# Kernel optimization log

Hardware: AMD Instinct MI355X
Metric: run time of the kernel (lower is better)

The kernel has to match this reference:

```python
import jax, jax.numpy as jnp
import numpy as np

LOCAL_RADIUS = 5


def setup_inputs() -> dict:
    key = jax.random.key(0)
    k1, k2, k3 = jax.random.split(key, 3)
    B, K, C, H = 4, 4096, 256, 128
    x = jax.random.normal(k1, (B, K, C), dtype=jnp.float32)
    W1 = jax.random.normal(k2, (C, H), dtype=jnp.float32) * (1.0 / np.sqrt(C))
    b1 = jnp.zeros((H,), dtype=jnp.float32)
    W2 = jax.random.normal(k3, (H, 1), dtype=jnp.float32) * (1.0 / np.sqrt(H))
    b2 = jnp.zeros((1,), dtype=jnp.float32)
    return {"x": x, "W1": W1, "b1": b1, "W2": W2, "b2": b2}


def reference(x, W1, b1, W2, b2):
    # x: [B, k, C]. The MLP score for column j is independent of the row i,
    # so compute it once per token instead of per (i, window) as in the torch loop.
    B, k, C = x.shape
    s = (jnp.tanh(x @ W1 + b1) @ W2 + b2)[..., 0]  # [B, k]
    idx = jnp.arange(k)
    band = (jnp.abs(idx[:, None] - idx[None, :]) <= LOCAL_RADIUS)  # [k, k]
    # Outside the band the original leaves scores at 0.0 (not -inf), so
    # out-of-window positions still contribute exp(0)=1 to the softmax.
    scores = jnp.where(band[None, :, :], s[:, None, :], jnp.float32(0.0))  # [B, k, k]
    weights = jax.nn.softmax(scores, axis=-1)  # [B, k, k]
    weighted = jnp.einsum('bij,bjc->bic', weights, x)  # [B, k, C]
    return weighted, weights
```

## Files before the change

kernel.cpp:

```cpp
#include <hip/hip_runtime.h>
#include <math.h>

#define B_ 4
#define K_ 4096
#define C_ 256
#define H_ 128
#define RAD 5
#define NB (2 * RAD + 1)
#define PSTRIDE 12

typedef float floatx4 __attribute__((ext_vector_type(4)));


__global__ __launch_bounds__(128) void score_kernel(
    const float* __restrict__ x, const float* __restrict__ W1,
    const float* __restrict__ b1, const float* __restrict__ W2,
    const float* __restrict__ b2, float* __restrict__ s_out)
{
    const int tid = threadIdx.x;
    const int t0 = blockIdx.x * 8;
    const float* xr[8];
    #pragma unroll
    for (int t = 0; t < 8; ++t) xr[t] = x + (size_t)(t0 + t) * C_;

    float acc[8];
    float binit = b1[tid];
    #pragma unroll
    for (int t = 0; t < 8; ++t) acc[t] = binit;

    for (int c = 0; c < C_; c += 4) {
        float w0 = W1[(c + 0) * H_ + tid];
        float w1 = W1[(c + 1) * H_ + tid];
        float w2 = W1[(c + 2) * H_ + tid];
        float w3 = W1[(c + 3) * H_ + tid];
        #pragma unroll
        for (int t = 0; t < 8; ++t) {
            floatx4 xv = *(const floatx4*)&xr[t][c];
            acc[t] = fmaf(xv.x, w0, acc[t]);
            acc[t] = fmaf(xv.y, w1, acc[t]);
            acc[t] = fmaf(xv.z, w2, acc[t]);
            acc[t] = fmaf(xv.w, w3, acc[t]);
        }
    }

    __shared__ float red[2][8];
    float w2v = W2[tid];
    #pragma unroll
    for (int t = 0; t < 8; ++t) {
        float p = tanhf(acc[t]) * w2v;
        #pragma unroll
        for (int off = 32; off > 0; off >>= 1) p += __shfl_down(p, off);
        if ((tid & 63) == 0) red[tid >> 6][t] = p;
    }
    __syncthreads();
    if (tid < 8) s_out[t0 + tid] = red[0][tid] + red[1][tid] + b2[0];
}

__global__ __launch_bounds__(256) void colsum_partial(
    const float* __restrict__ x, float* __restrict__ partial)
{
    const int tid = threadIdx.x;
    const int blk = blockIdx.x;
    const float* base = x + (size_t)blk * 32 * C_ + tid;
    float a0 = 0.f, a1 = 0.f, a2 = 0.f, a3 = 0.f;
    #pragma unroll
    for (int kk = 0; kk < 32; kk += 4) {
        a0 += base[(size_t)(kk + 0) * C_];
        a1 += base[(size_t)(kk + 1) * C_];
        a2 += base[(size_t)(kk + 2) * C_];
        a3 += base[(size_t)(kk + 3) * C_];
    }
    partial[(size_t)blk * C_ + tid] = (a0 + a1) + (a2 + a3);
}

__global__ __launch_bounds__(256) void colsum_final(
    const float* __restrict__ partial, float* __restrict__ Ssum)
{
    const int tid = threadIdx.x;
    const int b = blockIdx.x;
    float acc = 0.f;
    for (int chunk = 0; chunk < 128; ++chunk)
        acc += partial[(size_t)(b * 128 + chunk) * C_ + tid];
    Ssum[b * C_ + tid] = acc;
}

__global__ __launch_bounds__(256) void params_kernel(
    const float* __restrict__ s, float* __restrict__ params)
{
    const int row = blockIdx.x * 256 + threadIdx.x;
    const int b = row >> 12;
    const int i = row & (K_ - 1);
    const int j0 = max(0, i - RAD), j1 = min(K_ - 1, i + RAD);
    const int nb = j1 - j0 + 1;
    const float* srow = s + b * K_;

    float sv[NB];
    float m = 0.f;
    #pragma unroll
    for (int jj = 0; jj < NB; ++jj) {
        float v = (jj < nb) ? srow[j0 + jj] : 0.f;
        sv[jj] = v;
        if (jj < nb) m = fmaxf(m, v);
    }
    float e0 = expf(-m);
    float D = (float)(K_ - nb) * e0;
    float* pp = params + (size_t)row * PSTRIDE;
    #pragma unroll
    for (int jj = 0; jj < NB; ++jj) {
        float e = expf(sv[jj] - m);
        if (jj < nb) D += e;
        sv[jj] = e;
    }
    float inv = 1.0f / D;
    #pragma unroll
    for (int jj = 0; jj < NB; ++jj) pp[jj] = sv[jj] * inv;
    pp[11] = e0 * inv;
}

__global__ __launch_bounds__(256) void store_kernel(
    const float* __restrict__ x, const float* __restrict__ params,
    const float* __restrict__ Ssum, float* __restrict__ out)
{
    const int tid = threadIdx.x;
    const int row = blockIdx.x;
    const int b = row >> 12;
    const int i = row & (K_ - 1);
    const int j0 = max(0, i - RAD), j1 = min(K_ - 1, i + RAD);
    const int nb = j1 - j0 + 1;

    __shared__ float wbs[PSTRIDE];
    if (tid < PSTRIDE) wbs[tid] = params[(size_t)row * PSTRIDE + tid];
    __syncthreads();
    const float woff = wbs[11];

    {
        float acc = woff * Ssum[b * C_ + tid];
        const float* xb = x + ((size_t)b * K_ + j0) * C_ + tid;
        #pragma unroll
        for (int jj = 0; jj < NB; ++jj) {
            if (jj < nb)
                acc = fmaf(wbs[jj] - woff, xb[(size_t)jj * C_], acc);
        }
        out[(size_t)row * C_ + tid] = acc;
    }

    floatx4* wrow4 = (floatx4*)(out + (size_t)B_ * K_ * C_ + (size_t)row * K_);
    #pragma unroll
    for (int q = 0; q < 4; ++q) {
        const int f = tid + 256 * q;
        const int jb = f * 4;
        floatx4 v = { woff, woff, woff, woff };
        if (jb + 3 >= j0 && jb <= j1) {
            if (jb + 0 >= j0 && jb + 0 <= j1) v.x = wbs[jb + 0 - j0];
            if (jb + 1 >= j0 && jb + 1 <= j1) v.y = wbs[jb + 1 - j0];
            if (jb + 2 >= j0 && jb + 2 <= j1) v.z = wbs[jb + 2 - j0];
            if (jb + 3 >= j0 && jb + 3 <= j1) v.w = wbs[jb + 3 - j0];
        }
        __builtin_nontemporal_store(v, wrow4 + f);
    }
}

extern "C" void kernel_launch(void* const* d_in, const int* in_sizes, int n_in,
                              void* d_out, int out_size, void* d_ws, size_t ws_size,
                              hipStream_t stream) {
    const float* x  = (const float*)d_in[0];
    const float* W1 = (const float*)d_in[1];
    const float* b1 = (const float*)d_in[2];
    const float* W2 = (const float*)d_in[3];
    const float* b2 = (const float*)d_in[4];
    float* out = (float*)d_out;

    float* ws      = (float*)d_ws;
    float* s       = ws;
    float* Ssum    = ws + 16384;
    float* partial = ws + 17408;
    float* params  = ws + 148480;

    score_kernel  <<<B_ * K_ / 8,  128, 0, stream>>>(x, W1, b1, W2, b2, s);
    colsum_partial<<<B_ * 128,     256, 0, stream>>>(x, partial);
    colsum_final  <<<B_,           256, 0, stream>>>(partial, Ssum);
    params_kernel <<<B_ * K_ / 256,256, 0, stream>>>(s, params);
    store_kernel  <<<B_ * K_,      256, 0, stream>>>(x, params, Ssum, out);
}
```

Before: 380.3 us.

## Tile store kernel over 16 rows with shared x halo, parallelize colsum_final

The store kernel now handles 16 output rows per block. It stages the 26-token x window in shared memory once, so neighbouring rows reuse it instead of each re-reading 11 tokens from global memory. colsum_final goes from 256 to 1024 threads per block with a shared-memory reduction, shortening its serial loop. The weights matrix is now written with ordinary stores instead of nontemporal stores. That could change cache behaviour on the dominant 256 MB write stream and offset the savings.

Result: no change. 383.9 us (+0.9%).

```diff
diff --git a/kernel.cpp b/kernel.cpp
--- a/kernel.cpp
+++ b/kernel.cpp
@@ -8,6 +8,7 @@
 #define RAD 5
 #define NB (2 * RAD + 1)
 #define PSTRIDE 12
+#define TROWS 16
 
 typedef float floatx4 __attribute__((ext_vector_type(4)));
 
@@ -73,15 +74,20 @@
     partial[(size_t)blk * C_ + tid] = (a0 + a1) + (a2 + a3);
 }
 
-__global__ __launch_bounds__(256) void colsum_final(
+__global__ __launch_bounds__(1024) void colsum_final(
     const float* __restrict__ partial, float* __restrict__ Ssum)
 {
-    const int tid = threadIdx.x;
+    const int c = threadIdx.x & 255;
+    const int g = threadIdx.x >> 8;
     const int b = blockIdx.x;
+    __shared__ float red[4][C_];
     float acc = 0.f;
-    for (int chunk = 0; chunk < 128; ++chunk)
-        acc += partial[(size_t)(b * 128 + chunk) * C_ + tid];
-    Ssum[b * C_ + tid] = acc;
+    const float* pb = partial + ((size_t)b * 128 + g * 32) * C_ + c;
+    #pragma unroll 4
+    for (int ch = 0; ch < 32; ++ch) acc += pb[(size_t)ch * C_];
+    red[g][c] = acc;
+    __syncthreads();
+    if (g == 0) Ssum[b * C_ + c] = red[0][c] + red[1][c] + red[2][c] + red[3][c];
 }
 
 __global__ __launch_bounds__(256) void params_kernel(
@@ -117,46 +123,61 @@
     pp[11] = e0 * inv;
 }
 
-__global__ __launch_bounds__(256) void store_kernel(
+__global__ __launch_bounds__(256) void store16_kernel(
     const float* __restrict__ x, const float* __restrict__ params,
     const float* __restrict__ Ssum, float* __restrict__ out)
 {
     const int tid = threadIdx.x;
-    const int row = blockIdx.x;
-    const int b = row >> 12;
-    const int i = row & (K_ - 1);
-    const int j0 = max(0, i - RAD), j1 = min(K_ - 1, i + RAD);
-    const int nb = j1 - j0 + 1;
-
-    __shared__ float wbs[PSTRIDE];
-    if (tid < PSTRIDE) wbs[tid] = params[(size_t)row * PSTRIDE + tid];
+    const int blk = blockIdx.x;
+    const int b  = blk >> 8;
+    const int i0 = (blk & 255) * TROWS;
+
+    const int j0t = max(0, i0 - RAD);
+    const int j1t = min(K_ - 1, i0 + TROWS - 1 + RAD);
+    const int ntok = j1t - j0t + 1;
+
+    __shared__ float xs[TROWS + 2 * RAD][C_];
+    __shared__ float prm[TROWS][PSTRIDE];
+
+    if (tid < TROWS * PSTRIDE)
+        ((float*)prm)[tid] = params[(size_t)(b * K_ + i0) * PSTRIDE + tid];
+    const floatx4* xsrc = (const floatx4*)(x + ((size_t)b * K_ + j0t) * C_);
+    floatx4* xdst = (floatx4*)&xs[0][0];
+    for (int f = tid; f < ntok * (C_ / 4); f += 256) xdst[f] = xsrc[f];
     __syncthreads();
-    const float woff = wbs[11];
-
-    {
-        float acc = woff * Ssum[b * C_ + tid];
-        const float* xb = x + ((size_t)b * K_ + j0) * C_ + tid;
+
+    const float sc = Ssum[b * C_ + tid];
+    #pragma unroll
+    for (int r = 0; r < TROWS; ++r) {
+        const int i = i0 + r;
+        const int j0 = max(0, i - RAD), j1 = min(K_ - 1, i + RAD);
+        const float wo = prm[r][11];
+        float acc = wo * sc;
+        for (int j = j0; j <= j1; ++j)
+            acc = fmaf(prm[r][j - j0] - wo, xs[j - j0t][tid], acc);
+        out[((size_t)b * K_ + i) * C_ + tid] = acc;
+    }
+
+    float* wbase = out + (size_t)B_ * K_ * C_ + ((size_t)b * K_ + i0) * K_;
+    #pragma unroll
+    for (int r = 0; r < TROWS; ++r) {
+        const int i = i0 + r;
+        const int j0 = max(0, i - RAD), j1 = min(K_ - 1, i + RAD);
+        const float wo = prm[r][11];
+        floatx4* wrow4 = (floatx4*)(wbase + (size_t)r * K_);
         #pragma unroll
-        for (int jj = 0; jj < NB; ++jj) {
-            if (jj < nb)
-                acc = fmaf(wbs[jj] - woff, xb[(size_t)jj * C_], acc);
+        for (int q = 0; q < 4; ++q) {
+            const int f = tid + 256 * q;
+            const int jb = f * 4;
+            floatx4 v = { wo, wo, wo, wo };
+            if (jb + 3 >= j0 && jb <= j1) {
+                if (jb + 0 >= j0 && jb + 0 <= j1) v.x = prm[r][jb + 0 - j0];
+                if (jb + 1 >= j0 && jb + 1 <= j1) v.y = prm[r][jb + 1 - j0];
+                if (jb + 2 >= j0 && jb + 2 <= j1) v.z = prm[r][jb + 2 - j0];
+                if (jb + 3 >= j0 && jb + 3 <= j1) v.w = prm[r][jb + 3 - j0];
+            }
+            wrow4[f] = v;
         }
-        out[(size_t)row * C_ + tid] = acc;
-    }
-
-    floatx4* wrow4 = (floatx4*)(out + (size_t)B_ * K_ * C_ + (size_t)row * K_);
-    #pragma unroll
-    for (int q = 0; q < 4; ++q) {
-        const int f = tid + 256 * q;
-        const int jb = f * 4;
-        floatx4 v = { woff, woff, woff, woff };
-        if (jb + 3 >= j0 && jb <= j1) {
-            if (jb + 0 >= j0 && jb + 0 <= j1) v.x = wbs[jb + 0 - j0];
-            if (jb + 1 >= j0 && jb + 1 <= j1) v.y = wbs[jb + 1 - j0];
-            if (jb + 2 >= j0 && jb + 2 <= j1) v.z = wbs[jb + 2 - j0];
-            if (jb + 3 >= j0 && jb + 3 <= j1) v.w = wbs[jb + 3 - j0];
-        }
-        __builtin_nontemporal_store(v, wrow4 + f);
     }
 }
 
@@ -176,9 +197,9 @@
     float* partial = ws + 17408;
     float* params  = ws + 148480;
 
-    score_kernel  <<<B_ * K_ / 8,  128, 0, stream>>>(x, W1, b1, W2, b2, s);
-    colsum_partial<<<B_ * 128,     256, 0, stream>>>(x, partial);
-    colsum_final  <<<B_,           256, 0, stream>>>(partial, Ssum);
-    params_kernel <<<B_ * K_ / 256,256, 0, stream>>>(s, params);
-    store_kernel  <<<B_ * K_,      256, 0, stream>>>(x, params, Ssum, out);
-}
+    score_kernel  <<<B_ * K_ / 8,      128,  0, stream>>>(x, W1, b1, W2, b2, s);
+    colsum_partial<<<B_ * 128,         256,  0, stream>>>(x, partial);
+    colsum_final  <<<B_,               1024, 0, stream>>>(partial, Ssum);
+    params_kernel <<<B_ * K_ / 256,    256,  0, stream>>>(s, params);
+    store16_kernel<<<B_ * K_ / TROWS,  256,  0, stream>>>(x, params, Ssum, out);
+}
```
